# Kernel tuning notes

Measured on AMD Instinct MI355X. Metric: run time of the kernel, lower is better.

Reference implementation:

```python
import jax, jax.numpy as jnp
import numpy as np

NUM_EXPERTS = 64
HIDDEN_DIM = 4096
TOPK = 8


def setup_inputs() -> dict:
    key = jax.random.key(0)
    kx, kw = jax.random.split(key)
    x = jax.random.normal(kx, (16384, HIDDEN_DIM), dtype=jnp.float32)
    # nn.Linear weight is [num_experts, hidden_dim], init N(0, 0.01)
    W = jax.random.normal(kw, (NUM_EXPERTS, HIDDEN_DIM), dtype=jnp.float32) * 0.01
    return {"x": x, "W": W}


def reference(x, W):
    # router logits: [T, E]
    router_logits = jnp.einsum('th,eh->te', x, W)
    score = jnp.clip(router_logits, -2.0, 2.0)
    # top-k over experts (no router_bias branch)
    topk_scores, topk_indices = jax.lax.top_k(score, TOPK)  # [T, K]
    topk_probs = jax.nn.softmax(topk_scores, axis=-1)
    # dispatch index computation (counting-sort style)
    flat = topk_indices.reshape(-1)                      # [T*K]
    indices = jnp.argsort(flat, stable=True).astype(jnp.int32)
    tokens_per_expert = jnp.bincount(flat, length=NUM_EXPERTS)
    group_indices = jnp.cumsum(tokens_per_expert).astype(jnp.int32)
    tokens_per_expert_f = tokens_per_expert.astype(jnp.float32)
    # load-balance loss
    mean_tokens = tokens_per_expert_f / tokens_per_expert_f.sum()
    mean_prob = jax.nn.softmax(router_logits, axis=-1).mean(axis=0)
    lb_loss = jnp.dot(mean_tokens, mean_prob) * NUM_EXPERTS
    # z-loss
    zl = jnp.mean(jax.scipy.special.logsumexp(router_logits, axis=-1) ** 2)
    return (router_logits, topk_probs, topk_indices, group_indices,
            indices, tokens_per_expert, lb_loss, zl)
```

## Files before the change

kernel.cpp:

```cpp
#include <hip/hip_runtime.h>
#include <hip/hip_bf16.h>
#include <math.h>

#define NTOK   16384
#define NEXP   64
#define HID    4096
#define KSEL   8
#define EPS    7.5e-5f
#define NSPLIT 4
#define KSZ    (HID / NSPLIT)
#define RB     512

typedef __attribute__((ext_vector_type(8))) short short8;
typedef __attribute__((ext_vector_type(4))) float f32x4;

#define O_LOGITS 0u
#define O_PROBS  1048576u
#define O_TIDX   1179648u
#define O_GROUP  1310720u
#define O_IDX    1310784u
#define O_TPE    1441856u
#define O_LB     1441920u
#define O_ZL     1441921u

#define W_LSQP    4096u
#define W_TPE     8192u
#define W_PST     12288u
#define W_EBASE   16384u
#define W_CBE     131072u
#define W_PREF    393216u
#define W_PSUM    655360u
#define W_FLAT    1048576u
#define W_RNK     1572864u
#define W_WF      2097152u
#define W_PART    4194304u
#define PART_STRIDE 1048576ull

__device__ __forceinline__ unsigned short f2bf(float f) {
  unsigned u = __float_as_uint(f);
  return (unsigned short)((u + 0x7fffu + ((u >> 16) & 1u)) >> 16);
}

__device__ __forceinline__ void gload16(const void* g, void* l) {
  __builtin_amdgcn_global_load_lds((const __attribute__((address_space(1))) unsigned int*)g,
                                   (__attribute__((address_space(3))) unsigned int*)l, 16, 0, 0);
}

__global__ __launch_bounds__(256) void k_prep(const float* __restrict__ w,
                                              short8* __restrict__ wf) {
  const int kk   = blockIdx.x;
  const int nb   = threadIdx.x >> 6;
  const int lane = threadIdx.x & 63;
  const int n    = nb * 16 + (lane & 15);
  const int kb   = kk * 32 + (lane >> 4) * 8;
  const float4* wp = (const float4*)(w + (size_t)n * HID + kb);
  float4 f0 = wp[0], f1 = wp[1];
  float fv[8] = {f0.x, f0.y, f0.z, f0.w, f1.x, f1.y, f1.z, f1.w};
  short8 hi, lo;
#pragma unroll
  for (int j = 0; j < 8; ++j) {
    unsigned short h = f2bf(fv[j]);
    hi[j] = (short)h;
    float r = fv[j] - __uint_as_float((unsigned)h << 16);
    lo[j] = (short)f2bf(r);
  }
  size_t base = ((size_t)(kk * 4 + nb) * 2) * 64 + lane;
  wf[base] = hi;
  wf[base + 64] = lo;
}

__global__ __launch_bounds__(256, 4) void k_gemm(const float* __restrict__ x,
                                                 const short8* __restrict__ wf,
                                                 float* __restrict__ part) {
  __shared__ short8 wl[2][512];
  const int tid  = threadIdx.x;
  const int wv   = tid >> 6;
  const int lane = tid & 63;
  const int t0   = blockIdx.x * 64;
  const int k0   = blockIdx.y * KSZ;
  const int row  = t0 + wv * 16 + (lane & 15);

  const float* xp = x + (size_t)row * HID + k0 + (lane >> 4) * 8;
  const short8* wbase = wf + (size_t)(k0 >> 5) * 512;

  auto stage = [&](int c, int b) {
    const short8* src = wbase + (size_t)c * 512;
#pragma unroll
    for (int r = 0; r < 2; ++r) {
      const int o = r * 256 + wv * 64;
      gload16(src + o + lane, &wl[b][o]);
    }
  };

  f32x4 acc[4] = {{0,0,0,0},{0,0,0,0},{0,0,0,0},{0,0,0,0}};

  stage(0, 0);
  __syncthreads();
  const int nch = KSZ >> 5;
  for (int c = 0; c < nch; ++c) {
    const int b = c & 1;
    if (c + 1 < nch) stage(c + 1, b ^ 1);

    const float4* xq = (const float4*)(xp + c * 32);
    float4 f0 = xq[0], f1 = xq[1];
    unsigned xb[8] = {__float_as_uint(f0.x), __float_as_uint(f0.y),
                      __float_as_uint(f0.z), __float_as_uint(f0.w),
                      __float_as_uint(f1.x), __float_as_uint(f1.y),
                      __float_as_uint(f1.z), __float_as_uint(f1.w)};
    union { unsigned u[4]; short8 s; } ua, ul;
#pragma unroll
    for (int p = 0; p < 4; ++p) {
      unsigned b0 = xb[2 * p], b1 = xb[2 * p + 1];
      ua.u[p] = __builtin_amdgcn_perm(b1, b0, 0x07060302u);
      float r0 = __uint_as_float(b0) - __uint_as_float(b0 & 0xffff0000u);
      float r1 = __uint_as_float(b1) - __uint_as_float(b1 & 0xffff0000u);
      unsigned t0b = __float_as_uint(r0), t1b = __float_as_uint(r1);
      t0b += 0x7fffu + ((t0b >> 16) & 1u);
      t1b += 0x7fffu + ((t1b >> 16) & 1u);
      ul.u[p] = __builtin_amdgcn_perm(t1b, t0b, 0x07060302u);
    }
    short8 ah = ua.s, al = ul.s;

#pragma unroll
    for (int nb = 0; nb < 4; ++nb) {
      short8 bh = wl[b][nb * 128 + lane];
      short8 bl = wl[b][nb * 128 + 64 + lane];
      acc[nb] = __builtin_amdgcn_mfma_f32_16x16x32_bf16(ah, bh, acc[nb], 0, 0, 0);
      acc[nb] = __builtin_amdgcn_mfma_f32_16x16x32_bf16(al, bh, acc[nb], 0, 0, 0);
      acc[nb] = __builtin_amdgcn_mfma_f32_16x16x32_bf16(ah, bl, acc[nb], 0, 0, 0);
    }
    __syncthreads();
  }

  float* p = part + (size_t)blockIdx.y * PART_STRIDE;
  const int mrow = t0 + wv * 16 + (lane >> 4) * 4;
  const int col  = lane & 15;
#pragma unroll
  for (int nb = 0; nb < 4; ++nb)
#pragma unroll
    for (int r = 0; r < 4; ++r)
      p[(size_t)(mrow + r) * 64 + nb * 16 + col] = acc[nb][r];
}

__global__ __launch_bounds__(256) void k_reduce(const float* __restrict__ part,
                                                float* __restrict__ out_logits) {
  unsigned i4 = blockIdx.x * 256u + threadIdx.x;
  const float4* p4 = (const float4*)part;
  float4 v = p4[i4];
#pragma unroll
  for (int s = 1; s < NSPLIT; ++s) {
    float4 a = p4[(size_t)s * (PART_STRIDE / 4) + i4];
    v.x += a.x; v.y += a.y; v.z += a.z; v.w += a.w;
  }
  ((float4*)out_logits)[i4] = v;
}

__global__ __launch_bounds__(256) void k_rowwise(const float* __restrict__ lg,
                                                 const float* __restrict__ x,
                                                 const float* __restrict__ w,
                                                 float* __restrict__ out,
                                                 float* __restrict__ psum,
                                                 float* __restrict__ lsqp,
                                                 int* __restrict__ flat,
                                                 int* __restrict__ rnk_g,
                                                 int* __restrict__ cbe) {
  __shared__ float tile[32][68];
  __shared__ float rmv[32], invv[32], val8s[32];
  __shared__ unsigned long long Bmask[64];
  __shared__ int   fl_rows[32];
  __shared__ int   fl_n;
  __shared__ unsigned long long candmask;
  __shared__ double cexact[64];
  const int bid  = blockIdx.x;
  const int tid  = threadIdx.x;
  const int wv   = tid >> 6;
  const int lane = tid & 63;
  const int t0   = bid * 32;
  if (tid == 0) fl_n = 0;

  {
    const size_t boff = (size_t)bid * 2048;
#pragma unroll
    for (int k = 0; k < 8; ++k) {
      int idx = k * 256 + tid;
      tile[idx >> 6][idx & 63] = lg[boff + idx];
    }
  }
  __syncthreads();

  if (wv == 1) {
    float l2 = 0.0f;
    if (lane < 32) {
      const int r = lane;
      float rm = -3.0e38f;
#pragma unroll
      for (int c4 = 0; c4 < 16; ++c4) {
        float4 f = *(float4*)&tile[r][c4 * 4];
        rm = fmaxf(rm, fmaxf(fmaxf(f.x, f.y), fmaxf(f.z, f.w)));
      }
      float se = 0.0f;
#pragma unroll
      for (int c4 = 0; c4 < 16; ++c4) {
        float4 f = *(float4*)&tile[r][c4 * 4];
        se += expf(f.x - rm) + expf(f.y - rm) + expf(f.z - rm) + expf(f.w - rm);
      }
      rmv[r] = rm; invv[r] = 1.0f / se;
      float lse = rm + logf(se);
      l2 = lse * lse;
    }
#pragma unroll
    for (int o = 32; o > 0; o >>= 1) l2 += __shfl_down(l2, o);
    if (lane == 0) lsqp[bid] = l2;
  }
  __syncthreads();

  unsigned long long chosen = 0ull;
  int myidx[8] = {0,0,0,0,0,0,0,0};
  if (wv == 0 && lane < 32) {
    const unsigned t = t0 + lane;
    float val[9]; int idx[9];
#pragma unroll
    for (int j = 0; j < 9; ++j) { val[j] = -3.0e38f; idx[j] = 0; }
    bool flag = false;
#pragma unroll
    for (int c4 = 0; c4 < 16; ++c4) {
      float4 f = *(float4*)&tile[lane][c4 * 4];
      float fe[4] = {f.x, f.y, f.z, f.w};
#pragma unroll
      for (int jj = 0; jj < 4; ++jj) {
        float v = fe[jj];
        flag = flag || (fabsf(fabsf(v) - 2.0f) < EPS);
        float c = fminf(fmaxf(v, -2.0f), 2.0f);
        int id = c4 * 4 + jj;
#pragma unroll
        for (int j = 0; j < 9; ++j) {
          bool sw = c > val[j];
          float tv = sw ? val[j] : c; int ti = sw ? idx[j] : id;
          val[j] = sw ? c : val[j];   idx[j] = sw ? id : idx[j];
          c = tv; id = ti;
        }
      }
    }
    val8s[lane] = val[8];
#pragma unroll
    for (int j = 0; j < 8; ++j) {
      float gap = val[j] - val[j + 1];
      bool bothclip = (val[j] == val[j + 1]) && (fabsf(val[j]) == 2.0f);
      flag = flag || (gap < EPS && !bothclip);
    }
    if (!flag) {
      float m = val[0], pe[8], sum = 0.0f;
#pragma unroll
      for (int j = 0; j < 8; ++j) { pe[j] = expf(val[j] - m); sum += pe[j]; }
      float inv = 1.0f / sum;
      *(float4*)&out[O_PROBS + (size_t)t * 8]     = make_float4(pe[0]*inv, pe[1]*inv, pe[2]*inv, pe[3]*inv);
      *(float4*)&out[O_PROBS + (size_t)t * 8 + 4] = make_float4(pe[4]*inv, pe[5]*inv, pe[6]*inv, pe[7]*inv);
      *(float4*)&out[O_TIDX + (size_t)t * 8]      = make_float4((float)idx[0], (float)idx[1], (float)idx[2], (float)idx[3]);
      *(float4*)&out[O_TIDX + (size_t)t * 8 + 4]  = make_float4((float)idx[4], (float)idx[5], (float)idx[6], (float)idx[7]);
      *(int4*)&flat[(size_t)t * 8]     = make_int4(idx[0], idx[1], idx[2], idx[3]);
      *(int4*)&flat[(size_t)t * 8 + 4] = make_int4(idx[4], idx[5], idx[6], idx[7]);
#pragma unroll
      for (int j = 0; j < 8; ++j) { myidx[j] = idx[j]; chosen |= 1ull << idx[j]; }
    } else {
      int sl = atomicAdd(&fl_n, 1);
      fl_rows[sl] = lane;
    }
  } else if (wv == 2 || wv == 3) {
    const int e = lane, half = wv - 2;
    float s = 0.0f;
#pragma unroll
    for (int r = 0; r < 16; ++r) {
      int rr = half * 16 + r;
      s += expf(tile[rr][e] - rmv[rr]) * invv[rr];
    }
    psum[(size_t)bid * 128 + half * 64 + e] = s;
  }
  __syncthreads();

  for (int i = 0; i < fl_n; ++i) {
    const int r = fl_rows[i];
    if (wv == 0) {
      float c = fminf(fmaxf(tile[r][lane], -2.0f), 2.0f);
      bool cnd = (c >= val8s[r] - 3.0f * EPS);
      unsigned long long m = __ballot(cnd);
      if (lane == 0) candmask = m;
    }
    __syncthreads();
    const unsigned long long m = candmask;
    const float* xr = x + (size_t)(t0 + r) * HID;
    {
      int ord = 0;
      for (int e = 0; e < 64; ++e) {
        if ((m >> e) & 1ull) {
          if ((ord & 3) == wv) {
            const float* wr = w + (size_t)e * HID;
            double p0 = 0.0, p1 = 0.0, p2 = 0.0, p3 = 0.0;
            const int kb = lane * 64;
            for (int k = kb; k < kb + 64; k += 4) {
              float4 xv = *(const float4*)&xr[k];
              float4 wv4 = *(const float4*)&wr[k];
              p0 = fma((double)xv.x, (double)wv4.x, p0);
              p1 = fma((double)xv.y, (double)wv4.y, p1);
              p2 = fma((double)xv.z, (double)wv4.z, p2);
              p3 = fma((double)xv.w, (double)wv4.w, p3);
            }
            double p = (p0 + p1) + (p2 + p3);
#pragma unroll
            for (int o = 32; o > 0; o >>= 1) p += __shfl_down(p, o);
            if (lane == 0) cexact[e] = fmin(fmax(p, -2.0), 2.0);
          }
          ord++;
        }
      }
    }
    __syncthreads();
    if (tid == r) {
      double val[8]; int idx[8];
#pragma unroll
      for (int j = 0; j < 8; ++j) { val[j] = -1.0e300; idx[j] = 0; }
      for (int e = 0; e < 64; ++e) {
        if (!((m >> e) & 1ull)) continue;
        double c = cexact[e];
        int id = e;
#pragma unroll
        for (int j = 0; j < 8; ++j) {
          bool sw = c > val[j];
          double tv = sw ? val[j] : c; int ti = sw ? idx[j] : id;
          val[j] = sw ? c : val[j];    idx[j] = sw ? id : idx[j];
          c = tv; id = ti;
        }
      }
      float mm = (float)val[0], pe[8], sum = 0.0f;
#pragma unroll
      for (int j = 0; j < 8; ++j) { pe[j] = expf((float)val[j] - mm); sum += pe[j]; }
      float inv = 1.0f / sum;
      const unsigned t = t0 + r;
      chosen = 0ull;
#pragma unroll
      for (int j = 0; j < 8; ++j) {
        out[O_PROBS + (size_t)t * 8 + j] = pe[j] * inv;
        out[O_TIDX  + (size_t)t * 8 + j] = (float)idx[j];
        flat[(size_t)t * 8 + j] = idx[j];
        myidx[j] = idx[j];
        chosen |= 1ull << idx[j];
      }
    }
    __syncthreads();
  }

  if (wv == 0) {
    for (int e = 0; e < 64; ++e) {
      unsigned long long b = __ballot((chosen >> e) & 1ull);
      if (lane == 0) Bmask[e] = b;
    }
    __builtin_amdgcn_wave_barrier();
    if (lane < 32) {
      const unsigned long long below = (lane == 0) ? 0ull : (~0ull >> (64 - lane));
      int rr[8];
#pragma unroll
      for (int j = 0; j < 8; ++j)
        rr[j] = (int)__popcll(Bmask[myidx[j]] & below);
      *(int4*)&rnk_g[(size_t)bid * 256 + lane * 8]     = make_int4(rr[0], rr[1], rr[2], rr[3]);
      *(int4*)&rnk_g[(size_t)bid * 256 + lane * 8 + 4] = make_int4(rr[4], rr[5], rr[6], rr[7]);
    }
    cbe[bid * 64 + lane] = (int)__popcll(Bmask[lane]);
  }
}

__global__ __launch_bounds__(256) void k_scan(const int* __restrict__ cbe,
                                              const float* __restrict__ psum,
                                              int* __restrict__ pref,
                                              int* __restrict__ tpe_g,
                                              float* __restrict__ pst_g) {
  __shared__ int   wsum[4];
  __shared__ float fsum[4];
  const int e = blockIdx.x;
  const int tid = threadIdx.x;
  const int wv = tid >> 6, lane = tid & 63;

  const int c0 = cbe[(2 * tid) * 64 + e];
  const int c1 = cbe[(2 * tid + 1) * 64 + e];
  const int s = c0 + c1;

  int incl = s;
#pragma unroll
  for (int o = 1; o < 64; o <<= 1) {
    int n = __shfl_up(incl, o);
    if (lane >= o) incl += n;
  }
  if (lane == 63) wsum[wv] = incl;
  __syncthreads();
  int add = 0;
#pragma unroll
  for (int i = 0; i < 4; ++i) add += (i < wv) ? wsum[i] : 0;
  incl += add;
  const int excl = incl - s;
  pref[(2 * tid) * 64 + e]     = excl;
  pref[(2 * tid + 1) * 64 + e] = excl + c0;
  if (tid == 255) tpe_g[e] = incl;

  float p = psum[(size_t)(2 * tid) * 128 + e]     + psum[(size_t)(2 * tid) * 128 + 64 + e]
          + psum[(size_t)(2 * tid + 1) * 128 + e] + psum[(size_t)(2 * tid + 1) * 128 + 64 + e];
#pragma unroll
  for (int o = 32; o > 0; o >>= 1) p += __shfl_down(p, o);
  if (lane == 0) fsum[wv] = p;
  __syncthreads();
  if (tid == 0) pst_g[e] = (fsum[0] + fsum[1]) + (fsum[2] + fsum[3]);
}

__global__ __launch_bounds__(256) void k_fin(const int* __restrict__ tpe_g,
                                             const float* __restrict__ pst_g,
                                             const float* __restrict__ lsqp,
                                             int* __restrict__ ebase,
                                             float* __restrict__ out) {
  __shared__ float zbuf[4];
  const int tid = threadIdx.x;
  const int wv = tid >> 6, lane = tid & 63;

  float z = lsqp[tid] + lsqp[256 + tid];
#pragma unroll
  for (int o = 32; o > 0; o >>= 1) z += __shfl_down(z, o);
  if (lane == 0) zbuf[wv] = z;
  __syncthreads();
  if (tid == 0) out[O_ZL] = ((zbuf[0] + zbuf[1]) + (zbuf[2] + zbuf[3])) / 16384.0f;

  if (tid < 64) {
    int incl = 0;
    for (int i = 0; i <= tid; ++i) incl += tpe_g[i];
    const int tpe = tpe_g[tid];
    out[O_TPE + tid]   = (float)tpe;
    out[O_GROUP + tid] = (float)incl;
    ebase[tid] = incl - tpe;
    float term = ((float)tpe / 131072.0f) * (pst_g[tid] / 16384.0f) * 64.0f;
#pragma unroll
    for (int o = 32; o > 0; o >>= 1) term += __shfl_down(term, o);
    if (tid == 0) out[O_LB] = term;
  }
}

__global__ __launch_bounds__(256) void k_scatter(const int* __restrict__ flat,
                                                 const int* __restrict__ rnk,
                                                 const int* __restrict__ pref,
                                                 const int* __restrict__ ebase,
                                                 float* __restrict__ out) {
  const int j = blockIdx.x * 256 + threadIdx.x;
  const int e = flat[j];
  const int pos = ebase[e] + pref[(j >> 8) * 64 + e] + rnk[j];
  out[O_IDX + pos] = (float)j;
}

extern "C" void kernel_launch(void* const* d_in, const int* in_sizes, int n_in,
                              void* d_out, int out_size, void* d_ws, size_t ws_size,
                              hipStream_t stream) {
  (void)in_sizes; (void)n_in; (void)out_size; (void)ws_size;
  const float* x  = (const float*)d_in[0];
  const float* Wm = (const float*)d_in[1];
  float* out = (float*)d_out;
  char*  ws  = (char*)d_ws;

  float*  lsqp   = (float*)(ws + W_LSQP);
  int*    tpe_g  = (int*)(ws + W_TPE);
  float*  pst_g  = (float*)(ws + W_PST);
  int*    ebase  = (int*)(ws + W_EBASE);
  int*    cbe    = (int*)(ws + W_CBE);
  int*    pref   = (int*)(ws + W_PREF);
  float*  psum   = (float*)(ws + W_PSUM);
  int*    flat   = (int*)(ws + W_FLAT);
  int*    rnk    = (int*)(ws + W_RNK);
  short8* wf     = (short8*)(ws + W_WF);
  float*  part   = (float*)(ws + W_PART);

  k_prep   <<<dim3(128),  dim3(256), 0, stream>>>(Wm, wf);
  k_gemm   <<<dim3(NTOK / 64, NSPLIT), dim3(256), 0, stream>>>(x, wf, part);
  k_reduce <<<dim3(1024), dim3(256), 0, stream>>>(part, out + O_LOGITS);
  k_rowwise<<<dim3(RB),   dim3(256), 0, stream>>>(out + O_LOGITS, x, Wm, out, psum, lsqp, flat, rnk, cbe);
  k_scan   <<<dim3(64),   dim3(256), 0, stream>>>(cbe, psum, pref, tpe_g, pst_g);
  k_fin    <<<dim3(1),    dim3(256), 0, stream>>>(tpe_g, pst_g, lsqp, ebase, out);
  k_scatter<<<dim3(512),  dim3(256), 0, stream>>>(flat, rnk, pref, ebase, out);
}
```

Baseline: 151.5 us.

## Process 64 tokens per rowwise block and use fast exp/log intrinsics

The rowwise kernel now handles 64 tokens per block instead of 32, so every lane of the top-k and logsumexp wavefronts is active and the block count halves to 256. The scan, finalize and scatter kernels are adjusted to the coarser per-block counts, and the workspace layout is repacked to match. expf/logf are replaced with __expf/__logf, which trades accuracy for cheaper transcendentals. The risks are fewer blocks to spread across CUs and possible precision drift in the probabilities and loss outputs.

After: 141.1 us (median of 2 runs). 1.07x faster.

```diff
diff --git a/kernel.cpp b/kernel.cpp
--- a/kernel.cpp
+++ b/kernel.cpp
@@ -9,7 +9,6 @@
 #define EPS    7.5e-5f
 #define NSPLIT 4
 #define KSZ    (HID / NSPLIT)
-#define RB     512
 
 typedef __attribute__((ext_vector_type(8))) short short8;
 typedef __attribute__((ext_vector_type(4))) float f32x4;
@@ -24,14 +23,14 @@
 #define O_ZL     1441921u
 
 #define W_LSQP    4096u
-#define W_TPE     8192u
-#define W_PST     12288u
-#define W_EBASE   16384u
-#define W_CBE     131072u
-#define W_PREF    393216u
-#define W_PSUM    655360u
-#define W_FLAT    1048576u
-#define W_RNK     1572864u
+#define W_CBE     8192u
+#define W_PREF    73728u
+#define W_TPE     139264u
+#define W_PST     139520u
+#define W_EBASE   139776u
+#define W_PSUM    262144u
+#define W_FLAT    524288u
+#define W_RNK     1048576u
 #define W_WF      2097152u
 #define W_PART    4194304u
 #define PART_STRIDE 1048576ull
@@ -164,10 +163,10 @@
                                                  int* __restrict__ flat,
                                                  int* __restrict__ rnk_g,
                                                  int* __restrict__ cbe) {
-  __shared__ float tile[32][68];
-  __shared__ float rmv[32], invv[32], val8s[32];
+  __shared__ float tile[64][68];
+  __shared__ float rmv[64], invv[64], val8s[64];
   __shared__ unsigned long long Bmask[64];
-  __shared__ int   fl_rows[32];
+  __shared__ int   fl_rows[64];
   __shared__ int   fl_n;
   __shared__ unsigned long long candmask;
   __shared__ double cexact[64];
@@ -175,13 +174,13 @@
   const int tid  = threadIdx.x;
   const int wv   = tid >> 6;
   const int lane = tid & 63;
-  const int t0   = bid * 32;
+  const int t0   = bid * 64;
   if (tid == 0) fl_n = 0;
 
   {
-    const size_t boff = (size_t)bid * 2048;
-#pragma unroll
-    for (int k = 0; k < 8; ++k) {
+    const size_t boff = (size_t)bid * 4096;
+#pragma unroll
+    for (int k = 0; k < 16; ++k) {
       int idx = k * 256 + tid;
       tile[idx >> 6][idx & 63] = lg[boff + idx];
     }
@@ -189,25 +188,22 @@
   __syncthreads();
 
   if (wv == 1) {
-    float l2 = 0.0f;
-    if (lane < 32) {
-      const int r = lane;
-      float rm = -3.0e38f;
-#pragma unroll
-      for (int c4 = 0; c4 < 16; ++c4) {
-        float4 f = *(float4*)&tile[r][c4 * 4];
-        rm = fmaxf(rm, fmaxf(fmaxf(f.x, f.y), fmaxf(f.z, f.w)));
-      }
-      float se = 0.0f;
-#pragma unroll
-      for (int c4 = 0; c4 < 16; ++c4) {
-        float4 f = *(float4*)&tile[r][c4 * 4];
-        se += expf(f.x - rm) + expf(f.y - rm) + expf(f.z - rm) + expf(f.w - rm);
-      }
-      rmv[r] = rm; invv[r] = 1.0f / se;
-      float lse = rm + logf(se);
-      l2 = lse * lse;
-    }
+    const int r = lane;
+    float rm = -3.0e38f;
+#pragma unroll
+    for (int c4 = 0; c4 < 16; ++c4) {
+      float4 f = *(float4*)&tile[r][c4 * 4];
+      rm = fmaxf(rm, fmaxf(fmaxf(f.x, f.y), fmaxf(f.z, f.w)));
+    }
+    float se = 0.0f;
+#pragma unroll
+    for (int c4 = 0; c4 < 16; ++c4) {
+      float4 f = *(float4*)&tile[r][c4 * 4];
+      se += __expf(f.x - rm) + __expf(f.y - rm) + __expf(f.z - rm) + __expf(f.w - rm);
+    }
+    rmv[r] = rm; invv[r] = 1.0f / se;
+    float lse = rm + __logf(se);
+    float l2 = lse * lse;
 #pragma unroll
     for (int o = 32; o > 0; o >>= 1) l2 += __shfl_down(l2, o);
     if (lane == 0) lsqp[bid] = l2;
@@ -216,7 +212,7 @@
 
   unsigned long long chosen = 0ull;
   int myidx[8] = {0,0,0,0,0,0,0,0};
-  if (wv == 0 && lane < 32) {
+  if (wv == 0) {
     const unsigned t = t0 + lane;
     float val[9]; int idx[9];
 #pragma unroll
@@ -251,7 +247,7 @@
     if (!flag) {
       float m = val[0], pe[8], sum = 0.0f;
 #pragma unroll
-      for (int j = 0; j < 8; ++j) { pe[j] = expf(val[j] - m); sum += pe[j]; }
+      for (int j = 0; j < 8; ++j) { pe[j] = __expf(val[j] - m); sum += pe[j]; }
       float inv = 1.0f / sum;
       *(float4*)&out[O_PROBS + (size_t)t * 8]     = make_float4(pe[0]*inv, pe[1]*inv, pe[2]*inv, pe[3]*inv);
       *(float4*)&out[O_PROBS + (size_t)t * 8 + 4] = make_float4(pe[4]*inv, pe[5]*inv, pe[6]*inv, pe[7]*inv);
@@ -269,9 +265,9 @@
     const int e = lane, half = wv - 2;
     float s = 0.0f;
 #pragma unroll
-    for (int r = 0; r < 16; ++r) {
-      int rr = half * 16 + r;
-      s += expf(tile[rr][e] - rmv[rr]) * invv[rr];
+    for (int r = 0; r < 32; ++r) {
+      int rr = half * 32 + r;
+      s += __expf(tile[rr][e] - rmv[rr]) * invv[rr];
     }
     psum[(size_t)bid * 128 + half * 64 + e] = s;
   }
@@ -332,7 +328,7 @@
       }
       float mm = (float)val[0], pe[8], sum = 0.0f;
 #pragma unroll
-      for (int j = 0; j < 8; ++j) { pe[j] = expf((float)val[j] - mm); sum += pe[j]; }
+      for (int j = 0; j < 8; ++j) { pe[j] = __expf((float)val[j] - mm); sum += pe[j]; }
       float inv = 1.0f / sum;
       const unsigned t = t0 + r;
       chosen = 0ull;
@@ -354,15 +350,13 @@
       if (lane == 0) Bmask[e] = b;
     }
     __builtin_amdgcn_wave_barrier();
-    if (lane < 32) {
-      const unsigned long long below = (lane == 0) ? 0ull : (~0ull >> (64 - lane));
-      int rr[8];
-#pragma unroll
-      for (int j = 0; j < 8; ++j)
-        rr[j] = (int)__popcll(Bmask[myidx[j]] & below);
-      *(int4*)&rnk_g[(size_t)bid * 256 + lane * 8]     = make_int4(rr[0], rr[1], rr[2], rr[3]);
-      *(int4*)&rnk_g[(size_t)bid * 256 + lane * 8 + 4] = make_int4(rr[4], rr[5], rr[6], rr[7]);
-    }
+    const unsigned long long below = (lane == 0) ? 0ull : (~0ull >> (64 - lane));
+    int rr[8];
+#pragma unroll
+    for (int j = 0; j < 8; ++j)
+      rr[j] = (int)__popcll(Bmask[myidx[j]] & below);
+    *(int4*)&rnk_g[(size_t)bid * 512 + lane * 8]     = make_int4(rr[0], rr[1], rr[2], rr[3]);
+    *(int4*)&rnk_g[(size_t)bid * 512 + lane * 8 + 4] = make_int4(rr[4], rr[5], rr[6], rr[7]);
     cbe[bid * 64 + lane] = (int)__popcll(Bmask[lane]);
   }
 }
@@ -378,11 +372,8 @@
   const int tid = threadIdx.x;
   const int wv = tid >> 6, lane = tid & 63;
 
-  const int c0 = cbe[(2 * tid) * 64 + e];
-  const int c1 = cbe[(2 * tid + 1) * 64 + e];
-  const int s = c0 + c1;
-
-  int incl = s;
+  const int c = cbe[tid * 64 + e];
+  int incl = c;
 #pragma unroll
   for (int o = 1; o < 64; o <<= 1) {
     int n = __shfl_up(incl, o);
@@ -394,13 +385,10 @@
 #pragma unroll
   for (int i = 0; i < 4; ++i) add += (i < wv) ? wsum[i] : 0;
   incl += add;
-  const int excl = incl - s;
-  pref[(2 * tid) * 64 + e]     = excl;
-  pref[(2 * tid + 1) * 64 + e] = excl + c0;
+  pref[tid * 64 + e] = incl - c;
   if (tid == 255) tpe_g[e] = incl;
 
-  float p = psum[(size_t)(2 * tid) * 128 + e]     + psum[(size_t)(2 * tid) * 128 + 64 + e]
-          + psum[(size_t)(2 * tid + 1) * 128 + e] + psum[(size_t)(2 * tid + 1) * 128 + 64 + e];
+  float p = psum[(size_t)tid * 128 + e] + psum[(size_t)tid * 128 + 64 + e];
 #pragma unroll
   for (int o = 32; o > 0; o >>= 1) p += __shfl_down(p, o);
   if (lane == 0) fsum[wv] = p;
@@ -417,7 +405,7 @@
   const int tid = threadIdx.x;
   const int wv = tid >> 6, lane = tid & 63;
 
-  float z = lsqp[tid] + lsqp[256 + tid];
+  float z = lsqp[tid];
 #pragma unroll
   for (int o = 32; o > 0; o >>= 1) z += __shfl_down(z, o);
   if (lane == 0) zbuf[wv] = z;
@@ -445,7 +433,7 @@
                                                  float* __restrict__ out) {
   const int j = blockIdx.x * 256 + threadIdx.x;
   const int e = flat[j];
-  const int pos = ebase[e] + pref[(j >> 8) * 64 + e] + rnk[j];
+  const int pos = ebase[e] + pref[(j >> 9) * 64 + e] + rnk[j];
   out[O_IDX + pos] = (float)j;
 }
 
@@ -459,11 +447,11 @@
   char*  ws  = (char*)d_ws;
 
   float*  lsqp   = (float*)(ws + W_LSQP);
+  int*    cbe    = (int*)(ws + W_CBE);
+  int*    pref   = (int*)(ws + W_PREF);
   int*    tpe_g  = (int*)(ws + W_TPE);
   float*  pst_g  = (float*)(ws + W_PST);
   int*    ebase  = (int*)(ws + W_EBASE);
-  int*    cbe    = (int*)(ws + W_CBE);
-  int*    pref   = (int*)(ws + W_PREF);
   float*  psum   = (float*)(ws + W_PSUM);
   int*    flat   = (int*)(ws + W_FLAT);
   int*    rnk    = (int*)(ws + W_RNK);
@@ -473,7 +461,7 @@
   k_prep   <<<dim3(128),  dim3(256), 0, stream>>>(Wm, wf);
   k_gemm   <<<dim3(NTOK / 64, NSPLIT), dim3(256), 0, stream>>>(x, wf, part);
   k_reduce <<<dim3(1024), dim3(256), 0, stream>>>(part, out + O_LOGITS);
-  k_rowwise<<<dim3(RB),   dim3(256), 0, stream>>>(out + O_LOGITS, x, Wm, out, psum, lsqp, flat, rnk, cbe);
+  k_rowwise<<<dim3(256),  dim3(256), 0, stream>>>(out + O_LOGITS, x, Wm, out, psum, lsqp, flat, rnk, cbe);
   k_scan   <<<dim3(64),   dim3(256), 0, stream>>>(cbe, psum, pref, tpe_g, pst_g);
   k_fin    <<<dim3(1),    dim3(256), 0, stream>>>(tpe_g, pst_g, lsqp, ebase, out);
   k_scatter<<<dim3(512),  dim3(256), 0, stream>>>(flat, rnk, pref, ebase, out);
```
